# Performance work log

Hardware: AMD Instinct MI355X
Metric: run time of the kernel (lower is better)

## Reference

```python
import math
import jax, jax.numpy as jnp
import numpy as np

B, S, HID = 1, 2048, 4096
NH, NKV, D = 32, 8, 128
THETA = 10000.0


def setup_inputs() -> dict:
    key = jax.random.key(0)
    k1, k2, k3, k4, k5 = jax.random.split(key, 5)
    hidden_states = jax.random.normal(k1, (B, S, HID), dtype=jnp.float32)
    k_cache = jax.random.normal(k2, (B, NKV, S, D), dtype=jnp.float32)
    v_cache = jax.random.normal(k3, (B, NKV, S, D), dtype=jnp.float32)
    Wq = jax.random.normal(k4, (HID, NH * D), dtype=jnp.float32) * 0.02
    Wo = jax.random.normal(k5, (NH * D, HID), dtype=jnp.float32) * 0.02
    position_ids = jnp.broadcast_to(jnp.arange(S, dtype=jnp.int32), (B, S))
    # causal mask: True = masked out (torch.where(mask, -10000, scores))
    attention_mask = jnp.broadcast_to(
        jnp.triu(jnp.ones((S, S), dtype=bool), k=1)[None, None], (B, 1, S, S)
    )
    return {
        "hidden_states": hidden_states,
        "k_cache": k_cache,
        "v_cache": v_cache,
        "Wq": Wq,
        "Wo": Wo,
        "position_ids": position_ids,
        "attention_mask": attention_mask,
    }


def _rotate_half(x):
    x1, x2 = jnp.split(x, 2, axis=-1)
    return jnp.concatenate([-x2, x1], axis=-1)


def _rope_tables(position_ids):
    # Llama rotary embedding gathered at position_ids -> [B, 1, S, D]
    inv_freq = 1.0 / (THETA ** (jnp.arange(0, D, 2, dtype=jnp.float32) / D))
    freqs = position_ids[..., None].astype(jnp.float32) * inv_freq  # [B, S, D/2]
    emb = jnp.concatenate([freqs, freqs], axis=-1)  # [B, S, D]
    return jnp.cos(emb)[:, None], jnp.sin(emb)[:, None]


def reference(hidden_states, k_cache, v_cache, Wq, Wo, position_ids, attention_mask):
    G = NH // NKV  # GQA group size
    # q projection: [B, S, HID] -> [B, NH, S, D]
    q = (hidden_states @ Wq).reshape(B, S, NH, D).transpose(0, 2, 1, 3)
    cos, sin = _rope_tables(position_ids)
    q = q * cos + _rotate_half(q) * sin
    # GQA without materializing repeat_kv: group query heads over kv heads
    qg = q.reshape(B, NKV, G, S, D)
    scores = jnp.einsum("bkgsd,bktd->bkgst", qg, k_cache) / math.sqrt(D)
    scores = scores.reshape(B, NH, S, S)
    scores = jnp.where(attention_mask, jnp.float32(-10000.0), scores)
    probs = jax.nn.softmax(scores.astype(jnp.float32), axis=-1).astype(q.dtype)
    out = jnp.einsum("bkgst,bktd->bkgsd", probs.reshape(B, NKV, G, S, S), v_cache)
    out = out.reshape(B, NH, S, D).transpose(0, 2, 1, 3).reshape(B, S, NH * D)
    return out @ Wo
```

## Files before the change

### kernel.cpp

```cpp
#include <hip/hip_runtime.h>
#include <cstdint>
#include <cstddef>

#define S_LEN 2048
#define HID 4096
#define NH 32
#define NKV 8
#define HD 128

typedef __attribute__((ext_vector_type(4))) float f32x4;
typedef __attribute__((ext_vector_type(8))) short bf16x8;

__device__ __forceinline__ unsigned short f2bf(float f) {
  union { float f; uint32_t u; } v; v.f = f;
  uint32_t r = v.u + 0x7FFFu + ((v.u >> 16) & 1u);
  return (unsigned short)(r >> 16);
}

__global__ void cvt_bf16_kernel(const float* __restrict__ in,
                                unsigned short* __restrict__ out, int n4) {
  int i = blockIdx.x * blockDim.x + threadIdx.x;
  if (i >= n4) return;
  float4 v = ((const float4*)in)[i];
  ushort4 o;
  o.x = f2bf(v.x); o.y = f2bf(v.y); o.z = f2bf(v.z); o.w = f2bf(v.w);
  ((ushort4*)out)[i] = o;
}

__global__ void transpose_cvt_kernel(const float* __restrict__ in,
                                     unsigned short* __restrict__ out,
                                     int R, int C) {
  __shared__ float tile[32][33];
  const int b = blockIdx.z;
  const float* inb = in + (size_t)b * R * C;
  unsigned short* outb = out + (size_t)b * R * C;
  const int c0 = blockIdx.x * 32, r0 = blockIdx.y * 32;
  const int tx = threadIdx.x, ty = threadIdx.y;
#pragma unroll
  for (int i = ty; i < 32; i += 8)
    tile[i][tx] = inb[(size_t)(r0 + i) * C + (c0 + tx)];
  __syncthreads();
#pragma unroll
  for (int i = ty; i < 32; i += 8)
    outb[(size_t)(c0 + i) * R + (r0 + tx)] = f2bf(tile[tx][i]);
}

__global__ __launch_bounds__(256, 2) void gemm_bt_kernel(
    const unsigned short* __restrict__ A, const unsigned short* __restrict__ BT,
    float* __restrict__ C, int M, int N, int K) {
  __shared__ __align__(16) unsigned short As[128 * 32];
  __shared__ __align__(16) unsigned short Bs[128 * 32];
  const int tid = threadIdx.x;
  const int lane = tid & 63;
  const int wid = tid >> 6;
  const int wm = (wid >> 1) * 64, wn = (wid & 1) * 64;
  const int m0 = blockIdx.x * 128, n0 = blockIdx.y * 128;
  const int lr = lane & 15;
  const int q8 = (lane >> 4) << 3;
  f32x4 acc[4][4] = {};
  for (int kt = 0; kt < K; kt += 32) {
    __syncthreads();
#pragma unroll
    for (int p = 0; p < 2; ++p) {
      const int c = p * 256 + tid;
      const int r = c >> 2, off = (c & 3) << 3;
      __builtin_amdgcn_global_load_lds(
          (const __attribute__((address_space(1))) void*)(A + (size_t)(m0 + r) * K + kt + off),
          (__attribute__((address_space(3))) void*)(As + c * 8), 16, 0, 0);
      __builtin_amdgcn_global_load_lds(
          (const __attribute__((address_space(1))) void*)(BT + (size_t)(n0 + r) * K + kt + off),
          (__attribute__((address_space(3))) void*)(Bs + c * 8), 16, 0, 0);
    }
    __syncthreads();
    bf16x8 a[4], b[4];
#pragma unroll
    for (int t = 0; t < 4; ++t) {
      a[t] = *(const bf16x8*)(As + (wm + t * 16 + lr) * 32 + q8);
      b[t] = *(const bf16x8*)(Bs + (wn + t * 16 + lr) * 32 + q8);
    }
#pragma unroll
    for (int mt = 0; mt < 4; ++mt)
#pragma unroll
      for (int nt = 0; nt < 4; ++nt)
        acc[mt][nt] = __builtin_amdgcn_mfma_f32_16x16x32_bf16(a[mt], b[nt], acc[mt][nt], 0, 0, 0);
  }
  const int qd = (lane >> 4) << 2;
#pragma unroll
  for (int mt = 0; mt < 4; ++mt)
#pragma unroll
    for (int nt = 0; nt < 4; ++nt) {
      const int row = m0 + wm + mt * 16 + qd;
      const int col = n0 + wn + nt * 16 + lr;
#pragma unroll
      for (int r = 0; r < 4; ++r)
        C[(size_t)(row + r) * N + col] = acc[mt][nt][r];
    }
}

__global__ __launch_bounds__(256, 2) void gemm_rope_kernel(
    const unsigned short* __restrict__ A, const unsigned short* __restrict__ BT,
    const int* __restrict__ pos_ids, unsigned short* __restrict__ Qout) {
  __shared__ __align__(16) unsigned short As[128 * 32];
  __shared__ __align__(16) unsigned short Bs[128 * 32];
  const int tid = threadIdx.x;
  const int lane = tid & 63;
  const int wid = tid >> 6;
  const int wm = wid * 32;
  const int m0 = blockIdx.x * 128, n0 = blockIdx.y * 128;
  const int lr = lane & 15;
  const int q8 = (lane >> 4) << 3;
  f32x4 acc[2][8] = {};
  for (int kt = 0; kt < HID; kt += 32) {
    __syncthreads();
#pragma unroll
    for (int p = 0; p < 2; ++p) {
      const int c = p * 256 + tid;
      const int r = c >> 2, off = (c & 3) << 3;
      __builtin_amdgcn_global_load_lds(
          (const __attribute__((address_space(1))) void*)(A + (size_t)(m0 + r) * HID + kt + off),
          (__attribute__((address_space(3))) void*)(As + c * 8), 16, 0, 0);
      __builtin_amdgcn_global_load_lds(
          (const __attribute__((address_space(1))) void*)(BT + (size_t)(n0 + r) * HID + kt + off),
          (__attribute__((address_space(3))) void*)(Bs + c * 8), 16, 0, 0);
    }
    __syncthreads();
    bf16x8 a[2], b[8];
#pragma unroll
    for (int t = 0; t < 2; ++t)
      a[t] = *(const bf16x8*)(As + (wm + t * 16 + lr) * 32 + q8);
#pragma unroll
    for (int t = 0; t < 8; ++t)
      b[t] = *(const bf16x8*)(Bs + (t * 16 + lr) * 32 + q8);
#pragma unroll
    for (int mt = 0; mt < 2; ++mt)
#pragma unroll
      for (int nt = 0; nt < 8; ++nt)
        acc[mt][nt] = __builtin_amdgcn_mfma_f32_16x16x32_bf16(a[mt], b[nt], acc[mt][nt], 0, 0, 0);
  }
  const int qd = (lane >> 4) << 2;
  const int h = n0 >> 7;
#pragma unroll
  for (int mt = 0; mt < 2; ++mt)
#pragma unroll
    for (int r = 0; r < 4; ++r) {
      const int row = m0 + wm + mt * 16 + qd + r;
      const float pos = (float)pos_ids[row];
#pragma unroll
      for (int nt = 0; nt < 4; ++nt) {
        const int i = nt * 16 + lr;
        const float invf = __expf(-(float)(2 * i) * (9.2103403719761836f / 128.0f));
        float sn, cs;
        __sincosf(pos * invf, &sn, &cs);
        const float x1 = acc[mt][nt][r], x2 = acc[mt][nt + 4][r];
        Qout[((size_t)h * S_LEN + row) * HD + i]      = f2bf(x1 * cs - x2 * sn);
        Qout[((size_t)h * S_LEN + row) * HD + i + 64] = f2bf(x2 * cs + x1 * sn);
      }
    }
}

__global__ __launch_bounds__(256, 2) void attn_kernel(
    const unsigned short* __restrict__ Q, const unsigned short* __restrict__ Kc,
    const unsigned short* __restrict__ VT, unsigned short* __restrict__ Aout) {
  __shared__ __align__(16) unsigned short Ks[128 * 136];
  __shared__ __align__(16) unsigned short Vs[128 * 136];
  const int tid = threadIdx.x, lane = tid & 63, wid = tid >> 6;
  const int qh = blockIdx.x;
  const int qt = (blockIdx.y < 8) ? (15 - (int)blockIdx.y) : ((int)blockIdx.y - 8);
  const int kvh = qh >> 2;
  const int lr = lane & 15, quad = lane >> 4;
  const float scale = 0.08838834764831843f;
  unsigned short* Pw = Ks + wid * (32 * 136);

  bf16x8 qf[2][4];
#pragma unroll
  for (int mt = 0; mt < 2; ++mt)
#pragma unroll
    for (int kk = 0; kk < 4; ++kk)
      qf[mt][kk] = *(const bf16x8*)(Q + ((size_t)qh * S_LEN + qt * 128 + wid * 32 + mt * 16 + lr) * HD + kk * 32 + quad * 8);

  f32x4 o[2][8] = {};
  float lsum[2][4] = {};

  for (int kt = 0; kt <= qt; ++kt) {
    __syncthreads();
#pragma unroll
    for (int p = 0; p < 8; ++p) {
      const int c = p * 256 + tid;
      const int r = c >> 4, off = (c & 15) << 3;
      *(bf16x8*)(Ks + r * 136 + off) = *(const bf16x8*)(Kc + ((size_t)kvh * S_LEN + kt * 128 + r) * HD + off);
      *(bf16x8*)(Vs + r * 136 + off) = *(const bf16x8*)(VT + ((size_t)kvh * HD + r) * S_LEN + kt * 128 + off);
    }
    __syncthreads();

    f32x4 sv[2][8];
#pragma unroll
    for (int mt = 0; mt < 2; ++mt)
#pragma unroll
      for (int nt = 0; nt < 8; ++nt) {
        f32x4 s = {};
#pragma unroll
        for (int kk = 0; kk < 4; ++kk) {
          bf16x8 kf = *(const bf16x8*)(Ks + (nt * 16 + lr) * 136 + kk * 32 + quad * 8);
          s = __builtin_amdgcn_mfma_f32_16x16x32_bf16(qf[mt][kk], kf, s, 0, 0, 0);
        }
        sv[mt][nt] = s;
      }
    __syncthreads();

    const bool diag = (kt == qt);
#pragma unroll
    for (int mt = 0; mt < 2; ++mt)
#pragma unroll
      for (int r = 0; r < 4; ++r) {
        const int qrow = qt * 128 + wid * 32 + mt * 16 + quad * 4 + r;
        float ls = 0.f;
#pragma unroll
        for (int nt = 0; nt < 8; ++nt) {
          float v = sv[mt][nt][r] * scale - 16.0f;
          if (diag && (kt * 128 + nt * 16 + lr) > qrow) v = -1e30f;
          const float p = __expf(v);
          ls += p;
          Pw[(mt * 16 + quad * 4 + r) * 136 + nt * 16 + lr] = f2bf(p);
        }
        lsum[mt][r] += ls;
      }
    bf16x8 pf[2][4];
#pragma unroll
    for (int mt = 0; mt < 2; ++mt)
#pragma unroll
      for (int kk = 0; kk < 4; ++kk)
        pf[mt][kk] = *(const bf16x8*)(Pw + (mt * 16 + lr) * 136 + kk * 32 + quad * 8);
#pragma unroll
    for (int dt = 0; dt < 8; ++dt)
#pragma unroll
      for (int kk = 0; kk < 4; ++kk) {
        bf16x8 vf = *(const bf16x8*)(Vs + (dt * 16 + lr) * 136 + kk * 32 + quad * 8);
        o[0][dt] = __builtin_amdgcn_mfma_f32_16x16x32_bf16(pf[0][kk], vf, o[0][dt], 0, 0, 0);
        o[1][dt] = __builtin_amdgcn_mfma_f32_16x16x32_bf16(pf[1][kk], vf, o[1][dt], 0, 0, 0);
      }
  }

#pragma unroll
  for (int mt = 0; mt < 2; ++mt)
#pragma unroll
    for (int r = 0; r < 4; ++r) {
      float l = lsum[mt][r];
#pragma unroll
      for (int sh = 1; sh < 16; sh <<= 1) l += __shfl_xor(l, sh);
      const float inv = 1.0f / l;
      const int qrow = qt * 128 + wid * 32 + mt * 16 + quad * 4 + r;
#pragma unroll
      for (int dt = 0; dt < 8; ++dt)
        Aout[(size_t)qrow * HID + qh * HD + dt * 16 + lr] = f2bf(o[mt][dt][r] * inv);
    }
}

extern "C" void kernel_launch(void* const* d_in, const int* in_sizes, int n_in,
                              void* d_out, int out_size, void* d_ws, size_t ws_size,
                              hipStream_t stream) {
  const float* hidden  = (const float*)d_in[0];
  const float* k_cache = (const float*)d_in[1];
  const float* v_cache = (const float*)d_in[2];
  const float* Wq      = (const float*)d_in[3];
  const float* Wo      = (const float*)d_in[4];
  const int*   pos     = (const int*)d_in[5];
  float* out = (float*)d_out;

  char* ws = (char*)d_ws;
  unsigned short* hidden_bf = (unsigned short*)(ws + 0);
  unsigned short* attn_bf   = hidden_bf;
  unsigned short* WqT       = (unsigned short*)(ws + 16777216);
  unsigned short* WoT       = (unsigned short*)(ws + 50331648);
  unsigned short* k_bf      = (unsigned short*)(ws + 83886080);
  unsigned short* vT        = (unsigned short*)(ws + 88080384);
  unsigned short* q_bf      = (unsigned short*)(ws + 92274688);

  cvt_bf16_kernel<<<(S_LEN * HID / 4 + 255) / 256, 256, 0, stream>>>(hidden, hidden_bf, S_LEN * HID / 4);
  cvt_bf16_kernel<<<(NKV * S_LEN * HD / 4 + 255) / 256, 256, 0, stream>>>(k_cache, k_bf, NKV * S_LEN * HD / 4);
  transpose_cvt_kernel<<<dim3(HID / 32, HID / 32, 1), dim3(32, 8), 0, stream>>>(Wq, WqT, HID, HID);
  transpose_cvt_kernel<<<dim3(HID / 32, HID / 32, 1), dim3(32, 8), 0, stream>>>(Wo, WoT, HID, HID);
  transpose_cvt_kernel<<<dim3(HD / 32, S_LEN / 32, NKV), dim3(32, 8), 0, stream>>>(v_cache, vT, S_LEN, HD);

  gemm_rope_kernel<<<dim3(S_LEN / 128, HID / 128), 256, 0, stream>>>(hidden_bf, WqT, pos, q_bf);

  attn_kernel<<<dim3(NH, S_LEN / 128), 256, 0, stream>>>(q_bf, k_bf, vT, attn_bf);

  gemm_bt_kernel<<<dim3(S_LEN / 128, HID / 128), 256, 0, stream>>>(attn_bf, WoT, out, S_LEN, HID, HID);
}
```

Baseline: 491.6 us.

## Widen transpose tiles, deepen GEMM K-tiles, remap blocks per XCD, prefetch attention K/V

The transpose-convert kernel now uses 64x64 tiles with float4 loads and 16-byte bf16 stores instead of scalar accesses. Both GEMMs double the K-step to 64, which halves the number of barriers per unit of work. They also use a 1D grid remapped so blocks sharing A rows land on the same XCD, aiming for better L2 reuse. The attention kernel prefetches the next K/V tile into registers while computing the current one. This raises LDS use and register pressure, which could hurt occupancy.

```diff
diff --git a/kernel.cpp b/kernel.cpp
--- a/kernel.cpp
+++ b/kernel.cpp
@@ -27,43 +27,54 @@
   ((ushort4*)out)[i] = o;
 }
 
-__global__ void transpose_cvt_kernel(const float* __restrict__ in,
-                                     unsigned short* __restrict__ out,
-                                     int R, int C) {
-  __shared__ float tile[32][33];
+__global__ __launch_bounds__(256) void transpose_cvt_kernel(
+    const float* __restrict__ in, unsigned short* __restrict__ out, int R, int C) {
+  __shared__ float tile[64][65];
   const int b = blockIdx.z;
   const float* inb = in + (size_t)b * R * C;
   unsigned short* outb = out + (size_t)b * R * C;
-  const int c0 = blockIdx.x * 32, r0 = blockIdx.y * 32;
-  const int tx = threadIdx.x, ty = threadIdx.y;
-#pragma unroll
-  for (int i = ty; i < 32; i += 8)
-    tile[i][tx] = inb[(size_t)(r0 + i) * C + (c0 + tx)];
+  const int c0 = blockIdx.x * 64, r0 = blockIdx.y * 64;
+  const int tid = threadIdx.x;
+#pragma unroll
+  for (int p = 0; p < 4; ++p) {
+    const int ch = p * 256 + tid;
+    const int r = ch >> 4, off = (ch & 15) << 2;
+    *(float4*)&tile[r][off] = *(const float4*)(inb + (size_t)(r0 + r) * C + c0 + off);
+  }
   __syncthreads();
 #pragma unroll
-  for (int i = ty; i < 32; i += 8)
-    outb[(size_t)(c0 + i) * R + (r0 + tx)] = f2bf(tile[tx][i]);
+  for (int p = 0; p < 2; ++p) {
+    const int ch = p * 256 + tid;
+    const int i = ch >> 3, j0 = (ch & 7) << 3;
+    bf16x8 v;
+#pragma unroll
+    for (int k = 0; k < 8; ++k) v[k] = (short)f2bf(tile[j0 + k][i]);
+    *(bf16x8*)(outb + (size_t)(c0 + i) * R + r0 + j0) = v;
+  }
 }
 
 __global__ __launch_bounds__(256, 2) void gemm_bt_kernel(
     const unsigned short* __restrict__ A, const unsigned short* __restrict__ BT,
     float* __restrict__ C, int M, int N, int K) {
-  __shared__ __align__(16) unsigned short As[128 * 32];
-  __shared__ __align__(16) unsigned short Bs[128 * 32];
+  __shared__ __align__(16) unsigned short As[128 * 64];
+  __shared__ __align__(16) unsigned short Bs[128 * 64];
   const int tid = threadIdx.x;
   const int lane = tid & 63;
   const int wid = tid >> 6;
   const int wm = (wid >> 1) * 64, wn = (wid & 1) * 64;
-  const int m0 = blockIdx.x * 128, n0 = blockIdx.y * 128;
+  const int g = blockIdx.x;
+  const int xcd = g & 7, local = g >> 3;
+  const int m0 = (xcd * 2 + (local & 1)) * 128;
+  const int n0 = (local >> 1) * 128;
   const int lr = lane & 15;
   const int q8 = (lane >> 4) << 3;
   f32x4 acc[4][4] = {};
-  for (int kt = 0; kt < K; kt += 32) {
-    __syncthreads();
-#pragma unroll
-    for (int p = 0; p < 2; ++p) {
+  for (int kt = 0; kt < K; kt += 64) {
+    __syncthreads();
+#pragma unroll
+    for (int p = 0; p < 4; ++p) {
       const int c = p * 256 + tid;
-      const int r = c >> 2, off = (c & 3) << 3;
+      const int r = c >> 3, off = (c & 7) << 3;
       __builtin_amdgcn_global_load_lds(
           (const __attribute__((address_space(1))) void*)(A + (size_t)(m0 + r) * K + kt + off),
           (__attribute__((address_space(3))) void*)(As + c * 8), 16, 0, 0);
@@ -72,17 +83,20 @@
           (__attribute__((address_space(3))) void*)(Bs + c * 8), 16, 0, 0);
     }
     __syncthreads();
-    bf16x8 a[4], b[4];
-#pragma unroll
-    for (int t = 0; t < 4; ++t) {
-      a[t] = *(const bf16x8*)(As + (wm + t * 16 + lr) * 32 + q8);
-      b[t] = *(const bf16x8*)(Bs + (wn + t * 16 + lr) * 32 + q8);
-    }
-#pragma unroll
-    for (int mt = 0; mt < 4; ++mt)
-#pragma unroll
-      for (int nt = 0; nt < 4; ++nt)
-        acc[mt][nt] = __builtin_amdgcn_mfma_f32_16x16x32_bf16(a[mt], b[nt], acc[mt][nt], 0, 0, 0);
+#pragma unroll
+    for (int h = 0; h < 2; ++h) {
+      bf16x8 a[4], b[4];
+#pragma unroll
+      for (int t = 0; t < 4; ++t) {
+        a[t] = *(const bf16x8*)(As + (wm + t * 16 + lr) * 64 + h * 32 + q8);
+        b[t] = *(const bf16x8*)(Bs + (wn + t * 16 + lr) * 64 + h * 32 + q8);
+      }
+#pragma unroll
+      for (int mt = 0; mt < 4; ++mt)
+#pragma unroll
+        for (int nt = 0; nt < 4; ++nt)
+          acc[mt][nt] = __builtin_amdgcn_mfma_f32_16x16x32_bf16(a[mt], b[nt], acc[mt][nt], 0, 0, 0);
+    }
   }
   const int qd = (lane >> 4) << 2;
 #pragma unroll
@@ -100,22 +114,25 @@
 __global__ __launch_bounds__(256, 2) void gemm_rope_kernel(
     const unsigned short* __restrict__ A, const unsigned short* __restrict__ BT,
     const int* __restrict__ pos_ids, unsigned short* __restrict__ Qout) {
-  __shared__ __align__(16) unsigned short As[128 * 32];
-  __shared__ __align__(16) unsigned short Bs[128 * 32];
+  __shared__ __align__(16) unsigned short As[128 * 64];
+  __shared__ __align__(16) unsigned short Bs[128 * 64];
   const int tid = threadIdx.x;
   const int lane = tid & 63;
   const int wid = tid >> 6;
   const int wm = wid * 32;
-  const int m0 = blockIdx.x * 128, n0 = blockIdx.y * 128;
+  const int g = blockIdx.x;
+  const int xcd = g & 7, local = g >> 3;
+  const int m0 = (xcd * 2 + (local & 1)) * 128;
+  const int n0 = (local >> 1) * 128;
   const int lr = lane & 15;
   const int q8 = (lane >> 4) << 3;
   f32x4 acc[2][8] = {};
-  for (int kt = 0; kt < HID; kt += 32) {
-    __syncthreads();
-#pragma unroll
-    for (int p = 0; p < 2; ++p) {
+  for (int kt = 0; kt < HID; kt += 64) {
+    __syncthreads();
+#pragma unroll
+    for (int p = 0; p < 4; ++p) {
       const int c = p * 256 + tid;
-      const int r = c >> 2, off = (c & 3) << 3;
+      const int r = c >> 3, off = (c & 7) << 3;
       __builtin_amdgcn_global_load_lds(
           (const __attribute__((address_space(1))) void*)(A + (size_t)(m0 + r) * HID + kt + off),
           (__attribute__((address_space(3))) void*)(As + c * 8), 16, 0, 0);
@@ -124,18 +141,21 @@
           (__attribute__((address_space(3))) void*)(Bs + c * 8), 16, 0, 0);
     }
     __syncthreads();
-    bf16x8 a[2], b[8];
-#pragma unroll
-    for (int t = 0; t < 2; ++t)
-      a[t] = *(const bf16x8*)(As + (wm + t * 16 + lr) * 32 + q8);
-#pragma unroll
-    for (int t = 0; t < 8; ++t)
-      b[t] = *(const bf16x8*)(Bs + (t * 16 + lr) * 32 + q8);
-#pragma unroll
-    for (int mt = 0; mt < 2; ++mt)
-#pragma unroll
-      for (int nt = 0; nt < 8; ++nt)
-        acc[mt][nt] = __builtin_amdgcn_mfma_f32_16x16x32_bf16(a[mt], b[nt], acc[mt][nt], 0, 0, 0);
+#pragma unroll
+    for (int h = 0; h < 2; ++h) {
+      bf16x8 a[2], b[8];
+#pragma unroll
+      for (int t = 0; t < 2; ++t)
+        a[t] = *(const bf16x8*)(As + (wm + t * 16 + lr) * 64 + h * 32 + q8);
+#pragma unroll
+      for (int t = 0; t < 8; ++t)
+        b[t] = *(const bf16x8*)(Bs + (t * 16 + lr) * 64 + h * 32 + q8);
+#pragma unroll
+      for (int mt = 0; mt < 2; ++mt)
+#pragma unroll
+        for (int nt = 0; nt < 8; ++nt)
+          acc[mt][nt] = __builtin_amdgcn_mfma_f32_16x16x32_bf16(a[mt], b[nt], acc[mt][nt], 0, 0, 0);
+    }
   }
   const int qd = (lane >> 4) << 2;
   const int h = n0 >> 7;
@@ -181,16 +201,32 @@
   f32x4 o[2][8] = {};
   float lsum[2][4] = {};
 
+  const int sr = tid >> 4, soff = (tid & 15) << 3;
+  bf16x8 kreg[8], vreg[8];
+#pragma unroll
+  for (int p = 0; p < 8; ++p) {
+    const int r = sr + p * 16;
+    kreg[p] = *(const bf16x8*)(Kc + ((size_t)kvh * S_LEN + 0 * 128 + r) * HD + soff);
+    vreg[p] = *(const bf16x8*)(VT + ((size_t)kvh * HD + r) * S_LEN + 0 * 128 + soff);
+  }
+
   for (int kt = 0; kt <= qt; ++kt) {
     __syncthreads();
 #pragma unroll
     for (int p = 0; p < 8; ++p) {
-      const int c = p * 256 + tid;
-      const int r = c >> 4, off = (c & 15) << 3;
-      *(bf16x8*)(Ks + r * 136 + off) = *(const bf16x8*)(Kc + ((size_t)kvh * S_LEN + kt * 128 + r) * HD + off);
-      *(bf16x8*)(Vs + r * 136 + off) = *(const bf16x8*)(VT + ((size_t)kvh * HD + r) * S_LEN + kt * 128 + off);
-    }
-    __syncthreads();
+      const int r = sr + p * 16;
+      *(bf16x8*)(Ks + r * 136 + soff) = kreg[p];
+      *(bf16x8*)(Vs + r * 136 + soff) = vreg[p];
+    }
+    __syncthreads();
+    if (kt < qt) {
+#pragma unroll
+      for (int p = 0; p < 8; ++p) {
+        const int r = sr + p * 16;
+        kreg[p] = *(const bf16x8*)(Kc + ((size_t)kvh * S_LEN + (kt + 1) * 128 + r) * HD + soff);
+        vreg[p] = *(const bf16x8*)(VT + ((size_t)kvh * HD + r) * S_LEN + (kt + 1) * 128 + soff);
+      }
+    }
 
     f32x4 sv[2][8];
 #pragma unroll
@@ -277,13 +313,13 @@
 
   cvt_bf16_kernel<<<(S_LEN * HID / 4 + 255) / 256, 256, 0, stream>>>(hidden, hidden_bf, S_LEN * HID / 4);
   cvt_bf16_kernel<<<(NKV * S_LEN * HD / 4 + 255) / 256, 256, 0, stream>>>(k_cache, k_bf, NKV * S_LEN * HD / 4);
-  transpose_cvt_kernel<<<dim3(HID / 32, HID / 32, 1), dim3(32, 8), 0, stream>>>(Wq, WqT, HID, HID);
-  transpose_cvt_kernel<<<dim3(HID / 32, HID / 32, 1), dim3(32, 8), 0, stream>>>(Wo, WoT, HID, HID);
-  transpose_cvt_kernel<<<dim3(HD / 32, S_LEN / 32, NKV), dim3(32, 8), 0, stream>>>(v_cache, vT, S_LEN, HD);
-
-  gemm_rope_kernel<<<dim3(S_LEN / 128, HID / 128), 256, 0, stream>>>(hidden_bf, WqT, pos, q_bf);
+  transpose_cvt_kernel<<<dim3(HID / 64, HID / 64, 1), 256, 0, stream>>>(Wq, WqT, HID, HID);
+  transpose_cvt_kernel<<<dim3(HID / 64, HID / 64, 1), 256, 0, stream>>>(Wo, WoT, HID, HID);
+  transpose_cvt_kernel<<<dim3(HD / 64, S_LEN / 64, NKV), 256, 0, stream>>>(v_cache, vT, S_LEN, HD);
+
+  gemm_rope_kernel<<<dim3((S_LEN / 128) * (HID / 128)), 256, 0, stream>>>(hidden_bf, WqT, pos, q_bf);
 
   attn_kernel<<<dim3(NH, S_LEN / 128), 256, 0, stream>>>(q_bf, k_bf, vT, attn_bf);
 
-  gemm_bt_kernel<<<dim3(S_LEN / 128, HID / 128), 256, 0, stream>>>(attn_bf, WoT, out, S_LEN, HID, HID);
-}
+  gemm_bt_kernel<<<dim3((S_LEN / 128) * (HID / 128)), 256, 0, stream>>>(attn_bf, WoT, out, S_LEN, HID, HID);
+}
```

New measurement: 637.4 us. +29.6%, slower.
